# Kernel optimization log

Measured on AMD Instinct MI355X. Metric: run time of the kernel, lower is better.

## Reference

```python
import jax, jax.numpy as jnp
import numpy as np

B, S, D, F, E = 8, 1024, 1024, 4096, 8
EPS = 1e-5  # fairseq LayerNorm default


def setup_inputs() -> dict:
    key = jax.random.key(0)
    ks = jax.random.split(key, 4)
    s = 0.02
    return {
        "input_features": jax.random.normal(ks[0], (B, S, D), jnp.float32),
        "centroids": jax.random.normal(ks[1], (E, D), jnp.float32) * 0.1,  # orthogonal_ gain=0.1 stand-in
        "ln_g": jnp.ones((E, D), jnp.float32),
        "ln_b": jnp.zeros((E, D), jnp.float32),
        "w1": jax.random.normal(ks[2], (E, D, F), jnp.float32) * s,
        "b1": jnp.zeros((E, F), jnp.float32),
        "w2": jax.random.normal(ks[3], (E, F, D), jnp.float32) * s,  # torch inits ff2 to zero; random here so bwd is non-trivial
        "b2": jnp.zeros((E, D), jnp.float32),
    }


def reference(input_features, centroids, ln_g, ln_b, w1, b1, w2, b2):
    # Single-worker inference path of BaseLayer: greedy top-1 routing, no shuffle,
    # All2All is the identity. sort_by_expert + per-expert blocks + inverse_sort
    # is equivalent to per-token routing, expressed here with a one-hot combine.
    x = input_features.reshape(-1, D)                         # [T, D] tokens
    aff = jax.lax.stop_gradient(x @ centroids.T)              # [T, E] affinities (torch.no_grad)
    eid = jnp.argmax(aff, axis=-1)                            # [T] greedy_assignment k=1

    # alpha = sigmoid(<token, its expert centroid>) -- grads DO flow to centroids here
    alpha = jax.nn.sigmoid(jnp.sum(x * centroids[eid], axis=-1, keepdims=True))  # [T, 1]

    # Per-expert LayerNorm: normalize once, gather per-token gamma/beta
    mu = jnp.mean(x, axis=-1, keepdims=True)
    var = jnp.mean((x - mu) ** 2, axis=-1, keepdims=True)
    xn = (x - mu) * jax.lax.rsqrt(var + EPS)
    xln = xn * ln_g[eid] + ln_b[eid]                          # [T, D]

    # BaseSublayer: xs + ff2(relu(ff1(LN(xs))))
    # combined with alpha gate: out = alpha*sub(x) + (1-alpha)*x = x + alpha*ffn_residual
    onehot = jax.nn.one_hot(eid, E, dtype=x.dtype)            # [T, E] dispatch mask
    ffn = jnp.zeros_like(x)
    for e in range(E):  # small fixed expert loop (structurally distinct weights)
        h = jax.nn.relu(xln @ w1[e] + b1[e])                  # [T, F]
        ffn = ffn + onehot[:, e:e + 1] * (h @ w2[e] + b2[e])  # [T, D]

    out = x + alpha * ffn
    return out.reshape(input_features.shape)
```

## Files before the change

kernel.cpp:

```cpp
#include <hip/hip_runtime.h>

#define NT 8192
#define DIM 1024
#define FDIM 4096
#define NEXP 8

typedef __attribute__((ext_vector_type(8))) short bfx8;
typedef __attribute__((ext_vector_type(4))) float fx4;

__device__ __forceinline__ unsigned short f2bf(float f) {
  union { float f; unsigned u; } v; v.f = f;
  unsigned u = v.u;
  unsigned r = u + 0x7FFFu + ((u >> 16) & 1u);
  return (unsigned short)(r >> 16);
}

__device__ __forceinline__ void gload16(const void* g, void* l) {
  __builtin_amdgcn_global_load_lds(
      (const __attribute__((address_space(1))) unsigned int*)g,
      (__attribute__((address_space(3))) unsigned int*)l, 16, 0, 0);
}

__device__ __forceinline__ void tr64_issue(
    const float* __restrict__ src, int C, int r0, int c0, float* T, int tid)
{
  const int lane = tid & 63, wv = tid >> 6;
  const int rw = wv * 4 + (lane >> 4);
#pragma unroll
  for (int i = 0; i < 4; ++i) {
    const int cb = (lane & 15) ^ (rw & 7) ^ (i * 2) ^ (rw >> 3);
    gload16(src + (size_t)(r0 + i * 16 + rw) * C + c0 + cb * 4,
            &T[(i * 16 + wv * 4) * 64]);
  }
}

__device__ __forceinline__ void tr64_process(
    unsigned short* __restrict__ dst, int R, int r0, int c0, const float* T, int tid)
{
  const int q = tid & 7, cy = tid >> 3;
#pragma unroll
  for (int it = 0; it < 2; ++it) {
    const int c = cy + it * 32;
    unsigned short o[8];
#pragma unroll
    for (int u = 0; u < 8; ++u)
      o[u] = f2bf(T[(q * 8 + u) * 64 + ((((c >> 2) ^ u ^ q) << 2) | (c & 3))]);
    *(uint4*)(dst + (size_t)(c0 + c) * R + r0 + q * 8) = *(const uint4*)o;
  }
}

__global__ void k_zero(int* __restrict__ counts) {
  if (threadIdx.x < NEXP) counts[threadIdx.x] = 0;
}

__global__ __launch_bounds__(256) void k_pre(
    const float* __restrict__ x, const float* __restrict__ cent,
    const float* __restrict__ g, const float* __restrict__ b,
    const float* __restrict__ w1,
    int* __restrict__ eid, float* __restrict__ alpha, int* __restrict__ counts,
    unsigned short* __restrict__ xln, unsigned short* __restrict__ w1t)
{
  __shared__ float T[64 * 64];
  __shared__ float part[4][NEXP], ps[4], pss[4];
  __shared__ float sMu, sRstd;
  __shared__ int sE;
  const int bid = blockIdx.x, tid = threadIdx.x;

  const int te = bid >> 10, trem = bid & 1023;
  const int tr0 = (trem & 15) * 64, tc0 = (trem >> 4) * 64;
  const float* tsrc = w1 + (size_t)te * DIM * FDIM;
  tr64_issue(tsrc, FDIM, tr0, tc0, T, tid);

  const int t = bid;
  const float4 xv = ((const float4*)(x + (size_t)t * DIM))[tid];
  float acc[NEXP];
#pragma unroll
  for (int e = 0; e < NEXP; ++e) {
    const float4 cv = ((const float4*)(cent + (size_t)e * DIM))[tid];
    acc[e] = xv.x * cv.x + xv.y * cv.y + xv.z * cv.z + xv.w * cv.w;
  }
  float s = xv.x + xv.y + xv.z + xv.w;
  float ss = xv.x * xv.x + xv.y * xv.y + xv.z * xv.z + xv.w * xv.w;
#pragma unroll
  for (int off = 32; off > 0; off >>= 1) {
#pragma unroll
    for (int e = 0; e < NEXP; ++e) acc[e] += __shfl_down(acc[e], off);
    s += __shfl_down(s, off); ss += __shfl_down(ss, off);
  }
  const int lane = tid & 63, w = tid >> 6;
  if (lane == 0) {
#pragma unroll
    for (int e = 0; e < NEXP; ++e) part[w][e] = acc[e];
    ps[w] = s; pss[w] = ss;
  }
  __syncthreads();
  if (tid == 0) {
    int best = 0; float bv = -1e30f;
#pragma unroll
    for (int e = 0; e < NEXP; ++e) {
      float v = part[0][e] + part[1][e] + part[2][e] + part[3][e];
      if (v > bv) { bv = v; best = e; }
    }
    eid[t] = best;
    alpha[t] = 1.0f / (1.0f + expf(-bv));
    atomicAdd(&counts[best], 1);
    const float sum = ps[0] + ps[1] + ps[2] + ps[3];
    const float sq  = pss[0] + pss[1] + pss[2] + pss[3];
    const float mu = sum * (1.0f / DIM);
    const float var = sq * (1.0f / DIM) - mu * mu;
    sE = best; sMu = mu; sRstd = rsqrtf(var + 1e-5f);
  }
  __syncthreads();
  const int e = sE;
  const float mu = sMu, rstd = sRstd;
  const float4 gv = ((const float4*)(g + (size_t)e * DIM))[tid];
  const float4 bv4 = ((const float4*)(b + (size_t)e * DIM))[tid];
  ushort4 o;
  o.x = f2bf((xv.x - mu) * rstd * gv.x + bv4.x);
  o.y = f2bf((xv.y - mu) * rstd * gv.y + bv4.y);
  o.z = f2bf((xv.z - mu) * rstd * gv.z + bv4.z);
  o.w = f2bf((xv.w - mu) * rstd * gv.w + bv4.w);
  ((ushort4*)(xln + (size_t)t * DIM))[tid] = o;

  tr64_process(w1t + (size_t)te * DIM * FDIM, DIM, tr0, tc0, T, tid);
}

__global__ void k_scan(const int* __restrict__ counts, int* __restrict__ bs, int* __restrict__ cur) {
  if (threadIdx.x == 0) {
    int s = 0;
    for (int e = 0; e < NEXP; ++e) { bs[e] = s; cur[e] = s; s += counts[e]; }
  }
}

__global__ void k_rowtok(const int* __restrict__ eid, int* __restrict__ cur,
                         int* __restrict__ row_tok) {
  const int t = blockIdx.x * 256 + threadIdx.x;
  const int e = eid[t];
  const int pos = atomicAdd(&cur[e], 1);
  row_tok[pos] = t;
}

__global__ __launch_bounds__(256) void k_gemm1(
    const unsigned short* __restrict__ A,
    const unsigned short* __restrict__ Bt,
    const float* __restrict__ bias,
    const int* __restrict__ bs, const int* __restrict__ counts,
    unsigned short* __restrict__ Hout,
    const int* __restrict__ row_tok,
    const float* __restrict__ w2, unsigned short* __restrict__ w2t)
{
  __shared__ __align__(16) char smem[32 * 132 * 4];
  const int tid = threadIdx.x;

  if (blockIdx.x >= 16384) {
    const int i = blockIdx.x - 16384, e = i >> 10, rem = i & 1023;
    float* T = (float*)smem;
    const float* src = w2 + (size_t)e * FDIM * DIM;
    unsigned short* dst = w2t + (size_t)e * FDIM * DIM;
    const int r0 = (rem >> 4) * 64, c0 = (rem & 15) * 64;
    tr64_issue(src, DIM, r0, c0, T, tid);
    __syncthreads();
    tr64_process(dst, FDIM, r0, c0, T, tid);
    return;
  }

  unsigned short* lA = (unsigned short*)smem;
  unsigned short* lB = (unsigned short*)(smem + 8192);
  float* Lf = (float*)smem;

  const int MB = NT / 128;
  const int bid = blockIdx.x;
  const int e = bid & 7;
  const int l = bid >> 3;
  const int m0 = (l % MB) * 128;
  const int cnt = counts[e];
  if (m0 >= cnt) return;
  const int n0 = (l / MB) * 128;
  const int rbase = bs[e];

  const int lane = tid & 63, wv = tid >> 6;
  const int wm = (wv >> 1) * 64, wn = (wv & 1) * 64;
  const int lr = lane & 15, lg = lane >> 4;

  fx4 acc[4][4] = {};

  const unsigned short* Bte = Bt + (size_t)e * (size_t)FDIM * DIM;

  const unsigned short* aP[2];
  const unsigned short* bP[2];
#pragma unroll
  for (int p = 0; p < 2; ++p) {
    const int g = p * 256 + tid;
    const int row = g >> 2, kq = (g & 3) * 8;
    int ar = rbase + m0 + row;
    ar = ar < NT ? ar : NT - 1;
    const int tok = row_tok[ar];
    aP[p] = A + (size_t)tok * DIM + kq;
    bP[p] = Bte + (size_t)(n0 + row) * DIM + kq;
  }

  for (int k0 = 0; k0 < DIM; k0 += 32) {
    gload16(aP[0] + k0, &lA[(0 * 4 + wv) * 512]);
    gload16(aP[1] + k0, &lA[(1 * 4 + wv) * 512]);
    gload16(bP[0] + k0, &lB[(0 * 4 + wv) * 512]);
    gload16(bP[1] + k0, &lB[(1 * 4 + wv) * 512]);
    __syncthreads();
    bfx8 bf[4];
#pragma unroll
    for (int j = 0; j < 4; ++j)
      bf[j] = *(const bfx8*)(&lB[(wn + j * 16 + lr) * 32 + lg * 8]);
#pragma unroll
    for (int i = 0; i < 4; ++i) {
      const bfx8 af = *(const bfx8*)(&lA[(wm + i * 16 + lr) * 32 + lg * 8]);
#pragma unroll
      for (int j = 0; j < 4; ++j)
        acc[i][j] = __builtin_amdgcn_mfma_f32_16x16x32_bf16(af, bf[j], acc[i][j], 0, 0, 0);
    }
    __syncthreads();
  }

  const float* be = bias + (size_t)e * FDIM;
  float bcol[4];
#pragma unroll
  for (int j = 0; j < 4; ++j) bcol[j] = be[n0 + wn + j * 16 + lr];

#pragma unroll
  for (int i = 0; i < 4; ++i) {
    __syncthreads();
#pragma unroll
    for (int r2 = 0; r2 < 4; ++r2) {
      const int rowp = (wv >> 1) * 16 + lg * 4 + r2;
#pragma unroll
      for (int j = 0; j < 4; ++j) {
        float v = acc[i][j][r2] + bcol[j];
        Lf[rowp * 132 + wn + j * 16 + lr] = v > 0.f ? v : 0.f;
      }
    }
    __syncthreads();
#pragma unroll
    for (int s = 0; s < 2; ++s) {
      const int tsk = tid + 256 * s;
      const int rr = tsk >> 4, cg = tsk & 15;
      const int ra = i * 16 + ((rr >> 4) << 6) + (rr & 15);
      if (m0 + ra < cnt) {
        const float4 a = *(const float4*)&Lf[rr * 132 + cg * 8];
        const float4 b = *(const float4*)&Lf[rr * 132 + cg * 8 + 4];
        unsigned short o[8] = { f2bf(a.x), f2bf(a.y), f2bf(a.z), f2bf(a.w),
                                f2bf(b.x), f2bf(b.y), f2bf(b.z), f2bf(b.w) };
        *(uint4*)(Hout + (size_t)(rbase + m0 + ra) * FDIM + n0 + cg * 8) =
            *(const uint4*)o;
      }
    }
  }
}

__global__ __launch_bounds__(256) void k_gemm2(
    const unsigned short* __restrict__ A,
    const unsigned short* __restrict__ Bt,
    const float* __restrict__ bias,
    const int* __restrict__ bs, const int* __restrict__ counts,
    const int* __restrict__ row_tok, const float* __restrict__ alpha,
    const float* __restrict__ xin, float* __restrict__ out)
{
  const int MB = NT / 128;
  const int bid = blockIdx.x;
  const int e = bid & 7;
  const int l = bid >> 3;
  const int m0 = (l % MB) * 128;
  const int cnt = counts[e];
  if (m0 >= cnt) return;
  const int n0 = (l / MB) * 128;
  const int rbase = bs[e];

  __shared__ __align__(16) char smem[32 * 132 * 4];
  unsigned short* lA = (unsigned short*)smem;
  unsigned short* lB = (unsigned short*)(smem + 8192);
  float* Lf = (float*)smem;

  const int tid = threadIdx.x;
  const int lane = tid & 63, wv = tid >> 6;
  const int wm = (wv >> 1) * 64, wn = (wv & 1) * 64;
  const int lr = lane & 15, lg = lane >> 4;

  fx4 acc[4][4] = {};

  const unsigned short* Bte = Bt + (size_t)e * (size_t)DIM * FDIM;

  const unsigned short* aP[2];
  const unsigned short* bP[2];
#pragma unroll
  for (int p = 0; p < 2; ++p) {
    const int g = p * 256 + tid;
    const int row = g >> 2, kq = (g & 3) * 8;
    int ar = rbase + m0 + row;
    ar = ar < NT ? ar : NT - 1;
    aP[p] = A + (size_t)ar * FDIM + kq;
    bP[p] = Bte + (size_t)(n0 + row) * FDIM + kq;
  }

  for (int k0 = 0; k0 < FDIM; k0 += 32) {
    gload16(aP[0] + k0, &lA[(0 * 4 + wv) * 512]);
    gload16(aP[1] + k0, &lA[(1 * 4 + wv) * 512]);
    gload16(bP[0] + k0, &lB[(0 * 4 + wv) * 512]);
    gload16(bP[1] + k0, &lB[(1 * 4 + wv) * 512]);
    __syncthreads();
    bfx8 bf[4];
#pragma unroll
    for (int j = 0; j < 4; ++j)
      bf[j] = *(const bfx8*)(&lB[(wn + j * 16 + lr) * 32 + lg * 8]);
#pragma unroll
    for (int i = 0; i < 4; ++i) {
      const bfx8 af = *(const bfx8*)(&lA[(wm + i * 16 + lr) * 32 + lg * 8]);
#pragma unroll
      for (int j = 0; j < 4; ++j)
        acc[i][j] = __builtin_amdgcn_mfma_f32_16x16x32_bf16(af, bf[j], acc[i][j], 0, 0, 0);
    }
    __syncthreads();
  }

  const float* be = bias + (size_t)e * DIM;
  float bcol[4];
#pragma unroll
  for (int j = 0; j < 4; ++j) bcol[j] = be[n0 + wn + j * 16 + lr];

#pragma unroll
  for (int i = 0; i < 4; ++i) {
    __syncthreads();
#pragma unroll
    for (int r2 = 0; r2 < 4; ++r2) {
      const int rowp = (wv >> 1) * 16 + lg * 4 + r2;
#pragma unroll
      for (int j = 0; j < 4; ++j)
        Lf[rowp * 132 + wn + j * 16 + lr] = acc[i][j][r2] + bcol[j];
    }
    __syncthreads();
#pragma unroll
    for (int s = 0; s < 4; ++s) {
      const int tsk = tid + 256 * s;
      const int rr = tsk >> 5, c4 = tsk & 31;
      const int ra = i * 16 + ((rr >> 4) << 6) + (rr & 15);
      if (m0 + ra < cnt) {
        const int tok = row_tok[rbase + m0 + ra];
        const float al = alpha[tok];
        const float4 v = *(const float4*)&Lf[rr * 132 + c4 * 4];
        const float4 xr = *(const float4*)(xin + (size_t)tok * DIM + n0 + c4 * 4);
        float4 o;
        o.x = xr.x + al * v.x;
        o.y = xr.y + al * v.y;
        o.z = xr.z + al * v.z;
        o.w = xr.w + al * v.w;
        *(float4*)(out + (size_t)tok * DIM + n0 + c4 * 4) = o;
      }
    }
  }
}

extern "C" void kernel_launch(void* const* d_in, const int* in_sizes, int n_in,
                              void* d_out, int out_size, void* d_ws, size_t ws_size,
                              hipStream_t stream)
{
  const float* x    = (const float*)d_in[0];
  const float* cent = (const float*)d_in[1];
  const float* ln_g = (const float*)d_in[2];
  const float* ln_b = (const float*)d_in[3];
  const float* w1   = (const float*)d_in[4];
  const float* b1   = (const float*)d_in[5];
  const float* w2   = (const float*)d_in[6];
  const float* b2   = (const float*)d_in[7];
  float* out = (float*)d_out;

  char* ws = (char*)d_ws;
  unsigned short* xln  = (unsigned short*)(ws);
  unsigned short* hbuf = (unsigned short*)(ws + (16ull << 20));
  unsigned short* w1t  = (unsigned short*)(ws + (80ull << 20));
  unsigned short* w2t  = (unsigned short*)(ws + (144ull << 20));
  char* tail = ws + (208ull << 20);
  int*    eid    = (int*)(tail);
  float*  alpha  = (float*)(tail + 32768);
  int*    rowtok = (int*)(tail + 65536);
  int*    counts = (int*)(tail + 98304);
  int*    basep  = counts + 16;
  int*    cur    = counts + 32;

  k_zero<<<1, 64, 0, stream>>>(counts);
  k_pre<<<NT, 256, 0, stream>>>(
      x, cent, ln_g, ln_b, w1, eid, alpha, counts, xln, w1t);
  k_scan<<<1, 1, 0, stream>>>(counts, basep, cur);
  k_rowtok<<<NT / 256, 256, 0, stream>>>(eid, cur, rowtok);
  k_gemm1<<<16384 + 8192, 256, 0, stream>>>(
      xln, w1t, b1, basep, counts, hbuf, rowtok, w2, w2t);
  k_gemm2<<<NEXP * (NT / 128) * (DIM / 128), 256, 0, stream>>>(
      hbuf, w2t, b2, basep, counts, rowtok, alpha, x, out);
}
```

Measured before the change: 412.6 us.

## Rewrite second expert GEMM with 256x128 tiles, double-buffered swizzled LDS pipeline

The second GEMM kernel moves to 512-thread blocks with 256x128 output tiles and a K step of 64. Global-to-LDS loads are double-buffered and interleaved with MFMA phases, using manual barriers, vmcnt waits and setprio. An XOR swizzle on the LDS layout is meant to avoid bank conflicts. The epilogue writes straight from registers, dropping the LDS staging. The goal is to hide load latency behind compute and raise data reuse, at the cost of one block per CU, a large LDS footprint and fragile hand-written waitcnt ordering.

```diff
diff --git a/kernel.cpp b/kernel.cpp
--- a/kernel.cpp
+++ b/kernel.cpp
@@ -254,7 +254,7 @@
   }
 }
 
-__global__ __launch_bounds__(256) void k_gemm2(
+__global__ __launch_bounds__(512, 1) void k_gemm2(
     const unsigned short* __restrict__ A,
     const unsigned short* __restrict__ Bt,
     const float* __restrict__ bias,
@@ -262,95 +262,112 @@
     const int* __restrict__ row_tok, const float* __restrict__ alpha,
     const float* __restrict__ xin, float* __restrict__ out)
 {
-  const int MB = NT / 128;
   const int bid = blockIdx.x;
   const int e = bid & 7;
   const int l = bid >> 3;
-  const int m0 = (l % MB) * 128;
+  const int m0 = (l & 31) * 256;
   const int cnt = counts[e];
   if (m0 >= cnt) return;
-  const int n0 = (l / MB) * 128;
+  const int n0 = (l >> 5) * 128;
   const int rbase = bs[e];
 
-  __shared__ __align__(16) char smem[32 * 132 * 4];
-  unsigned short* lA = (unsigned short*)smem;
-  unsigned short* lB = (unsigned short*)(smem + 8192);
-  float* Lf = (float*)smem;
+  __shared__ unsigned short sA[2][256 * 64];
+  __shared__ unsigned short sB[2][128 * 64];
 
   const int tid = threadIdx.x;
   const int lane = tid & 63, wv = tid >> 6;
-  const int wm = (wv >> 1) * 64, wn = (wv & 1) * 64;
   const int lr = lane & 15, lg = lane >> 4;
-
-  fx4 acc[4][4] = {};
+  const int sw = lr & 7;
+  const int brow = (wv * 16 + lr) * 64;
+
+  fx4 acc[16] = {};
 
   const unsigned short* Bte = Bt + (size_t)e * (size_t)DIM * FDIM;
 
-  const unsigned short* aP[2];
+  const unsigned short* aP[2][2];
+#pragma unroll
+  for (int h = 0; h < 2; ++h)
+#pragma unroll
+    for (int p = 0; p < 2; ++p) {
+      const int c = p * 512 + tid;
+      const int row = h * 128 + (c >> 3);
+      const int kq = ((c & 7) ^ ((c >> 3) & 7)) * 8;
+      int ar = rbase + m0 + row;
+      ar = ar < NT ? ar : NT - 1;
+      aP[h][p] = A + (size_t)ar * FDIM + kq;
+    }
   const unsigned short* bP[2];
 #pragma unroll
-  for (int p = 0; p < 2; ++p) {
-    const int g = p * 256 + tid;
-    const int row = g >> 2, kq = (g & 3) * 8;
-    int ar = rbase + m0 + row;
-    ar = ar < NT ? ar : NT - 1;
-    aP[p] = A + (size_t)ar * FDIM + kq;
-    bP[p] = Bte + (size_t)(n0 + row) * FDIM + kq;
-  }
-
-  for (int k0 = 0; k0 < FDIM; k0 += 32) {
-    gload16(aP[0] + k0, &lA[(0 * 4 + wv) * 512]);
-    gload16(aP[1] + k0, &lA[(1 * 4 + wv) * 512]);
-    gload16(bP[0] + k0, &lB[(0 * 4 + wv) * 512]);
-    gload16(bP[1] + k0, &lB[(1 * 4 + wv) * 512]);
-    __syncthreads();
-    bfx8 bf[4];
-#pragma unroll
-    for (int j = 0; j < 4; ++j)
-      bf[j] = *(const bfx8*)(&lB[(wn + j * 16 + lr) * 32 + lg * 8]);
-#pragma unroll
-    for (int i = 0; i < 4; ++i) {
-      const bfx8 af = *(const bfx8*)(&lA[(wm + i * 16 + lr) * 32 + lg * 8]);
-#pragma unroll
-      for (int j = 0; j < 4; ++j)
-        acc[i][j] = __builtin_amdgcn_mfma_f32_16x16x32_bf16(af, bf[j], acc[i][j], 0, 0, 0);
-    }
-    __syncthreads();
-  }
-
-  const float* be = bias + (size_t)e * DIM;
-  float bcol[4];
-#pragma unroll
-  for (int j = 0; j < 4; ++j) bcol[j] = be[n0 + wn + j * 16 + lr];
-
-#pragma unroll
-  for (int i = 0; i < 4; ++i) {
-    __syncthreads();
-#pragma unroll
-    for (int r2 = 0; r2 < 4; ++r2) {
-      const int rowp = (wv >> 1) * 16 + lg * 4 + r2;
-#pragma unroll
-      for (int j = 0; j < 4; ++j)
-        Lf[rowp * 132 + wn + j * 16 + lr] = acc[i][j][r2] + bcol[j];
-    }
-    __syncthreads();
-#pragma unroll
-    for (int s = 0; s < 4; ++s) {
-      const int tsk = tid + 256 * s;
-      const int rr = tsk >> 5, c4 = tsk & 31;
-      const int ra = i * 16 + ((rr >> 4) << 6) + (rr & 15);
-      if (m0 + ra < cnt) {
-        const int tok = row_tok[rbase + m0 + ra];
-        const float al = alpha[tok];
-        const float4 v = *(const float4*)&Lf[rr * 132 + c4 * 4];
-        const float4 xr = *(const float4*)(xin + (size_t)tok * DIM + n0 + c4 * 4);
-        float4 o;
-        o.x = xr.x + al * v.x;
-        o.y = xr.y + al * v.y;
-        o.z = xr.z + al * v.z;
-        o.w = xr.w + al * v.w;
-        *(float4*)(out + (size_t)tok * DIM + n0 + c4 * 4) = o;
-      }
+  for (int h = 0; h < 2; ++h) {
+    const int nrow = n0 + h * 64 + (tid >> 3);
+    const int kq = ((tid & 7) ^ ((tid >> 3) & 7)) * 8;
+    bP[h] = Bte + (size_t)nrow * FDIM + kq;
+  }
+
+#define SGA(bb, t, h) if ((t) < 64) {                                      \
+    gload16(aP[h][0] + (size_t)(t) * 64, &sA[bb][(h) * 8192 + wv * 512]);  \
+    gload16(aP[h][1] + (size_t)(t) * 64, &sA[bb][(h) * 8192 + 4096 + wv * 512]); }
+#define SGB(bb, t, h) if ((t) < 64) {                                      \
+    gload16(bP[h] + (size_t)(t) * 64, &sB[bb][(h) * 4096 + wv * 512]); }
+
+#define PH(ABUF, MH, BBUF, RDBF, STG, W)                                   \
+  {                                                                        \
+    bfx8 af0[8], af1[8];                                                   \
+    _Pragma("unroll")                                                      \
+    for (int j = 0; j < 8; ++j) {                                          \
+      const int ab = ((MH) * 8 + j) * 1024 + lr * 64;                      \
+      af0[j] = *(const bfx8*)&sA[ABUF][ab + ((lg ^ sw) << 3)];             \
+      af1[j] = *(const bfx8*)&sA[ABUF][ab + (((4 + lg) ^ sw) << 3)];       \
+    }                                                                      \
+    if (RDBF) {                                                            \
+      bf[0] = *(const bfx8*)&sB[BBUF][brow + ((lg ^ sw) << 3)];            \
+      bf[1] = *(const bfx8*)&sB[BBUF][brow + (((4 + lg) ^ sw) << 3)];      \
+    }                                                                      \
+    STG                                                                    \
+    asm volatile("s_barrier" ::: "memory");                                \
+    __builtin_amdgcn_s_setprio(1);                                         \
+    _Pragma("unroll")                                                      \
+    for (int j = 0; j < 8; ++j)                                            \
+      acc[(MH) * 8 + j] = __builtin_amdgcn_mfma_f32_16x16x32_bf16(         \
+          af0[j], bf[0], acc[(MH) * 8 + j], 0, 0, 0);                      \
+    _Pragma("unroll")                                                      \
+    for (int j = 0; j < 8; ++j)                                            \
+      acc[(MH) * 8 + j] = __builtin_amdgcn_mfma_f32_16x16x32_bf16(         \
+          af1[j], bf[1], acc[(MH) * 8 + j], 0, 0, 0);                      \
+    __builtin_amdgcn_s_setprio(0);                                         \
+    if (W) asm volatile("s_waitcnt vmcnt(2)" ::: "memory");                \
+    asm volatile("s_barrier" ::: "memory");                                \
+  }
+
+  bfx8 bf[2];
+
+  SGA(0, 0, 0) SGA(0, 0, 1) SGB(0, 0, 0) SGB(0, 0, 1) SGA(1, 1, 0)
+  asm volatile("s_waitcnt vmcnt(2)" ::: "memory");
+  asm volatile("s_barrier" ::: "memory");
+
+  for (int it = 0; it < 32; ++it) {
+    const int T0 = 2 * it, T1 = T0 + 1;
+    PH(0, 0, 0, 1, SGB(1, T1, 0) SGB(1, T1, 1), 0)
+    PH(0, 1, 0, 0, SGA(1, T1, 1) SGA(0, T0 + 2, 0), 1)
+    PH(1, 0, 1, 1, SGA(0, T0 + 2, 1) SGB(0, T0 + 2, 0), 0)
+    PH(1, 1, 1, 0, SGB(0, T0 + 2, 1) SGA(1, T1 + 2, 0), 1)
+  }
+#undef PH
+#undef SGA
+#undef SGB
+
+  const float bc = bias[(size_t)e * DIM + n0 + wv * 16 + lr];
+  const int col = n0 + wv * 16 + lr;
+#pragma unroll
+  for (int mi = 0; mi < 16; ++mi) {
+#pragma unroll
+    for (int r = 0; r < 4; ++r) {
+      const int row = mi * 16 + lg * 4 + r;
+      if (m0 + row >= cnt) continue;
+      const int tok = row_tok[rbase + m0 + row];
+      const float al = alpha[tok];
+      out[(size_t)tok * DIM + col] =
+          xin[(size_t)tok * DIM + col] + al * (acc[mi][r] + bc);
     }
   }
 }
@@ -389,6 +406,6 @@
   k_rowtok<<<NT / 256, 256, 0, stream>>>(eid, cur, rowtok);
   k_gemm1<<<16384 + 8192, 256, 0, stream>>>(
       xln, w1t, b1, basep, counts, hbuf, rowtok, w2, w2t);
-  k_gemm2<<<NEXP * (NT / 128) * (DIM / 128), 256, 0, stream>>>(
+  k_gemm2<<<NEXP * 32 * 8, 512, 0, stream>>>(
       hbuf, w2t, b2, basep, counts, rowtok, alpha, x, out);
 }
```

New measurement: 551.1 us. 33.6% more time.
